# Kernel tuning notes

Measured on AMD Instinct MI355X. Metric: run time of the kernel, lower is better.

Reference implementation:

```python
import jax, jax.numpy as jnp
import numpy as np

N_SEGMENT = 16
N_HEADS = 12
DIM = 768
HEAD_DIM = DIM // N_HEADS
LN_EPS = 1e-5


def setup_inputs() -> dict:
    key = jax.random.key(0)
    ks = jax.random.split(key, 12)
    nt, p, c = 512, 197, DIM
    s = 1.0 / np.sqrt(c)
    return {
        "x": jax.random.normal(ks[0], (nt, p, c), dtype=jnp.float32),
        "w1": jax.random.uniform(ks[1], (1, 1, c), dtype=jnp.float32) * 2.0 - 1.0,
        "ln_g": jnp.ones((c,), dtype=jnp.float32),
        "ln_b": jnp.zeros((c,), dtype=jnp.float32),
        "Wq": jax.random.normal(ks[2], (c, c), dtype=jnp.float32) * s,
        "bq": jax.random.normal(ks[3], (c,), dtype=jnp.float32) * 0.02,
        "Wk": jax.random.normal(ks[4], (c, c), dtype=jnp.float32) * s,
        "bk": jax.random.normal(ks[5], (c,), dtype=jnp.float32) * 0.02,
        "Wv": jax.random.normal(ks[6], (c, c), dtype=jnp.float32) * s,
        "bv": jax.random.normal(ks[7], (c,), dtype=jnp.float32) * 0.02,
        "Wo": jax.random.normal(ks[8], (c, c), dtype=jnp.float32) * s,
        "bo": jax.random.normal(ks[9], (c,), dtype=jnp.float32) * 0.02,
    }


def _layer_norm(x, g, b):
    mu = jnp.mean(x, axis=-1, keepdims=True)
    var = jnp.mean(jnp.square(x - mu), axis=-1, keepdims=True)
    return (x - mu) * jax.lax.rsqrt(var + LN_EPS) * g + b


def _attention(h, Wq, bq, Wk, bk, Wv, bv, Wo, bo):
    # h: [B, T, C]
    B, T, C = h.shape
    def heads(y):
        return y.reshape(B, T, N_HEADS, HEAD_DIM).transpose(0, 2, 1, 3)
    q = heads(h @ Wq + bq)  # [B, H, T, Dh]
    k = heads(h @ Wk + bk)
    v = heads(h @ Wv + bv)
    scores = jnp.einsum("bhtd,bhsd->bhts", q, k) / jnp.sqrt(jnp.float32(HEAD_DIM))
    probs = jax.nn.softmax(scores, axis=-1)
    ctx = jnp.einsum("bhts,bhsd->bhtd", probs, v)
    ctx = ctx.transpose(0, 2, 1, 3).reshape(B, T, C)
    return ctx @ Wo + bo


def reference(x, w1, ln_g, ln_b, Wq, bq, Wk, bk, Wv, bv, Wo, bo):
    nt, p, c = x.shape
    B = nt // N_SEGMENT
    xr = x.reshape(B, N_SEGMENT, p, c)
    s = xr[:, :, 0]  # CLS tokens [B, T, C]
    # weighted temporal shift (in torch this mutates the view; residual sees it)
    s_shift = s.at[:, 1:].add(s[:, :-1] * w1)
    t = _layer_norm(s_shift, ln_g, ln_b)
    t = _attention(t, Wq, bq, Wk, bk, Wv, bv, Wo, bo)
    t = t + s_shift  # residual uses SHIFTED tokens (aliasing in torch source)
    out = xr.at[:, :, 0].set(t)
    return out.reshape(nt, p, c)
```

## Files before the change

### kernel.cpp

```cpp
#include <hip/hip_runtime.h>
#include <math.h>

typedef __attribute__((ext_vector_type(8))) short short8;
typedef __attribute__((ext_vector_type(4))) float f32x4;
typedef __attribute__((ext_vector_type(4))) unsigned short us4;

constexpr int NSEG = 16;
constexpr int CC   = 768;
constexpr int PP   = 197;
constexpr int NH   = 12;
constexpr int HD   = 64;
constexpr int NT   = 512;
constexpr int MN   = NT * CC;
constexpr float LN_EPS = 1e-5f;

constexpr unsigned CPT  = 196 * CC / 4;
constexpr unsigned TOK4 = PP * CC / 4;
constexpr unsigned ROW4 = CC / 4;
constexpr unsigned W4TOT = (unsigned)NT * CPT;

__device__ inline unsigned short f2bf(float f) {
    unsigned u = __float_as_uint(f);
    u += 0x7fffu + ((u >> 16) & 1u);
    return (unsigned short)(u >> 16);
}

__device__ inline void copy_slice(const float* __restrict__ x, float* __restrict__ out,
                                  unsigned start, unsigned end,
                                  unsigned gthread, unsigned nthreads) {
    const float4* __restrict__ x4 = (const float4*)x;
    float4* __restrict__ o4 = (float4*)out;
    for (unsigned i = start + gthread; i < end; i += nthreads) {
        unsigned t = i / CPT;
        unsigned w = i - t * CPT;
        unsigned idx = t * TOK4 + ROW4 + w;
        o4[idx] = x4[idx];
    }
}

template<bool ADD_RES>
__device__ inline void gemm_tile(const unsigned short* __restrict__ A,
                                 const unsigned short* __restrict__ Bt,
                                 const float* __restrict__ bias,
                                 const float* __restrict__ res,
                                 float* __restrict__ outp,
                                 int by, int bx, size_t orow) {
    int tid  = threadIdx.x;
    int lane = tid & 63, wv = tid >> 6;
    int wr = wv >> 1, wc = wv & 1;
    int l15 = lane & 15, lh = lane >> 4;
    int m0 = by * 64 + wr * 32;
    int n0 = bx * 64 + wc * 32;
    f32x4 acc[2][2] = {};
    const unsigned short* Ar0 = A  + (size_t)(m0 + l15) * CC + lh * 8;
    const unsigned short* Ar1 = Ar0 + 16 * CC;
    const unsigned short* Br0 = Bt + (size_t)(n0 + l15) * CC + lh * 8;
    const unsigned short* Br1 = Br0 + 16 * CC;
    #pragma unroll 4
    for (int k0 = 0; k0 < CC; k0 += 32) {
        short8 a0 = *(const short8*)(Ar0 + k0);
        short8 a1 = *(const short8*)(Ar1 + k0);
        short8 b0 = *(const short8*)(Br0 + k0);
        short8 b1 = *(const short8*)(Br1 + k0);
        acc[0][0] = __builtin_amdgcn_mfma_f32_16x16x32_bf16(a0, b0, acc[0][0], 0, 0, 0);
        acc[0][1] = __builtin_amdgcn_mfma_f32_16x16x32_bf16(a0, b1, acc[0][1], 0, 0, 0);
        acc[1][0] = __builtin_amdgcn_mfma_f32_16x16x32_bf16(a1, b0, acc[1][0], 0, 0, 0);
        acc[1][1] = __builtin_amdgcn_mfma_f32_16x16x32_bf16(a1, b1, acc[1][1], 0, 0, 0);
    }
    #pragma unroll
    for (int mf = 0; mf < 2; ++mf)
        #pragma unroll
        for (int nf = 0; nf < 2; ++nf)
            #pragma unroll
            for (int r = 0; r < 4; ++r) {
                int row = m0 + mf * 16 + lh * 4 + r;
                int col = n0 + nf * 16 + l15;
                float v = acc[mf][nf][r] + bias[col];
                if (ADD_RES) v += res[(size_t)row * CC + col];
                outp[(size_t)row * orow + col] = v;
            }
}

constexpr int K1_LN = NT, K1_CVT = 2304, K1_CPY = 768;
__global__ __launch_bounds__(256) void k1(const float* __restrict__ x, const float* __restrict__ w1,
        const float* __restrict__ g, const float* __restrict__ bln,
        const float* __restrict__ Wq, const float* __restrict__ Wk,
        const float* __restrict__ Wv, const float* __restrict__ Wo,
        float* __restrict__ s_shift, unsigned short* __restrict__ tln,
        unsigned short* __restrict__ wt, float* __restrict__ out,
        unsigned cstart, unsigned cend) {
    __shared__ float smem[32 * 33];
    int bid = blockIdx.x, tid = threadIdx.x;
    if (bid < K1_LN) {
        int r = bid, seg = r & (NSEG - 1);
        float vals[3]; float local = 0.f;
        #pragma unroll
        for (int i = 0; i < 3; ++i) {
            int c = tid + i * 256;
            float v = x[(size_t)r * PP * CC + c];
            if (seg > 0) v += w1[c] * x[(size_t)(r - 1) * PP * CC + c];
            vals[i] = v; local += v;
        }
        smem[tid] = local; __syncthreads();
        for (int off = 128; off > 0; off >>= 1) {
            if (tid < off) smem[tid] += smem[tid + off];
            __syncthreads();
        }
        float mu = smem[0] * (1.0f / CC); __syncthreads();
        float lv = 0.f;
        #pragma unroll
        for (int i = 0; i < 3; ++i) { float d = vals[i] - mu; lv += d * d; }
        smem[tid] = lv; __syncthreads();
        for (int off = 128; off > 0; off >>= 1) {
            if (tid < off) smem[tid] += smem[tid + off];
            __syncthreads();
        }
        float rstd = rsqrtf(smem[0] * (1.0f / CC) + LN_EPS);
        #pragma unroll
        for (int i = 0; i < 3; ++i) {
            int c = tid + i * 256;
            s_shift[(size_t)r * CC + c] = vals[i];
            tln[(size_t)r * CC + c] = f2bf((vals[i] - mu) * rstd * g[c] + bln[c]);
        }
    } else if (bid < K1_LN + K1_CVT) {
        int idx = bid - K1_LN;
        int mat = idx / 576, tile = idx % 576;
        int tr = tile / 24, tc = tile % 24;
        const float* W = mat == 0 ? Wq : mat == 1 ? Wk : mat == 2 ? Wv : Wo;
        int lr = tid >> 3, lc = (tid & 7) * 4;
        float4 v = *(const float4*)(W + (size_t)(tr * 32 + lr) * CC + tc * 32 + lc);
        smem[lr * 33 + lc + 0] = v.x; smem[lr * 33 + lc + 1] = v.y;
        smem[lr * 33 + lc + 2] = v.z; smem[lr * 33 + lc + 3] = v.w;
        __syncthreads();
        int ln_ = tid >> 3, kc = (tid & 7) * 4;
        us4 o;
        #pragma unroll
        for (int j = 0; j < 4; ++j) o[j] = f2bf(smem[(kc + j) * 33 + ln_]);
        *(us4*)(wt + (size_t)mat * CC * CC + (size_t)(tc * 32 + ln_) * CC + tr * 32 + kc) = o;
    } else {
        unsigned cb = bid - (K1_LN + K1_CVT);
        copy_slice(x, out, cstart, cend, cb * 256 + tid, K1_CPY * 256);
    }
}

constexpr int K2_GEMM = 288, K2_CPY = 1024;
__global__ __launch_bounds__(256) void k2(const unsigned short* __restrict__ tln,
        const unsigned short* __restrict__ wt,
        const float* __restrict__ bq, const float* __restrict__ bk, const float* __restrict__ bv,
        float* __restrict__ qkv,
        const float* __restrict__ x, float* __restrict__ out,
        unsigned cstart, unsigned cend) {
    int bid = blockIdx.x, tid = threadIdx.x;
    if (bid < K2_GEMM) {
        int z = bid / 96, rem = bid % 96;
        int by = rem / 12, bx = rem % 12;
        const unsigned short* Bt = wt + (size_t)z * CC * CC;
        const float* bias = z == 0 ? bq : (z == 1 ? bk : bv);
        float* outp = qkv + (size_t)z * MN;
        gemm_tile<false>(tln, Bt, bias, nullptr, outp, by, bx, CC);
    } else {
        unsigned cb = bid - K2_GEMM;
        copy_slice(x, out, cstart, cend, cb * 256 + tid, K2_CPY * 256);
    }
}

constexpr int K3_ATT = 32 * NH, K3_CPY = 1024;
__global__ __launch_bounds__(256) void k3(const float* __restrict__ qkv,
        unsigned short* __restrict__ ctxb,
        const float* __restrict__ x, float* __restrict__ out,
        unsigned cstart, unsigned cend) {
    int bid = blockIdx.x, tid = threadIdx.x;
    if (bid < K3_ATT) {
        const float* q = qkv;
        const float* k = qkv + MN;
        const float* v = qkv + 2 * MN;
        int bb = bid / NH, h = bid % NH;
        __shared__ float qs[16][HD], ks[16][HD], vs[16][HD];
        __shared__ float sc[16][17];
        __shared__ float rsum[16];
        for (int i = tid; i < 16 * HD; i += 256) {
            int t = i >> 6, d = i & 63;
            size_t gidx = (size_t)(bb * NSEG + t) * CC + h * HD + d;
            qs[t][d] = q[gidx]; ks[t][d] = k[gidx]; vs[t][d] = v[gidx];
        }
        __syncthreads();
        {
            int t = tid >> 4, s = tid & 15;
            float acc = 0.f;
            #pragma unroll
            for (int d = 0; d < HD; ++d) acc += qs[t][d] * ks[s][d];
            sc[t][s] = acc * 0.125f;
        }
        __syncthreads();
        if (tid < 16) {
            float m = -1e30f;
            #pragma unroll
            for (int s = 0; s < 16; ++s) m = fmaxf(m, sc[tid][s]);
            float sum = 0.f;
            #pragma unroll
            for (int s = 0; s < 16; ++s) { float e = __expf(sc[tid][s] - m); sc[tid][s] = e; sum += e; }
            rsum[tid] = sum;
        }
        __syncthreads();
        for (int i = tid; i < 16 * HD; i += 256) {
            int t = i >> 6, d = i & 63;
            float acc = 0.f;
            #pragma unroll
            for (int s = 0; s < 16; ++s) acc += sc[t][s] * vs[s][d];
            ctxb[(size_t)(bb * NSEG + t) * CC + h * HD + d] = f2bf(acc / rsum[t]);
        }
    } else {
        unsigned cb = bid - K3_ATT;
        copy_slice(x, out, cstart, cend, cb * 256 + tid, K3_CPY * 256);
    }
}

constexpr int K4_GEMM = 96, K4_CPY = 1024;
__global__ __launch_bounds__(256) void k4(const unsigned short* __restrict__ ctxb,
        const unsigned short* __restrict__ wto,
        const float* __restrict__ bo, const float* __restrict__ s_shift,
        float* __restrict__ out, const float* __restrict__ x,
        unsigned cstart, unsigned cend) {
    int bid = blockIdx.x, tid = threadIdx.x;
    if (bid < K4_GEMM) {
        int by = bid / 12, bx = bid % 12;
        gemm_tile<true>(ctxb, wto, bo, s_shift, out, by, bx, (size_t)PP * CC);
    } else {
        unsigned cb = bid - K4_GEMM;
        copy_slice(x, out, cstart, cend, cb * 256 + tid, K4_CPY * 256);
    }
}

extern "C" void kernel_launch(void* const* d_in, const int* in_sizes, int n_in,
                              void* d_out, int out_size, void* d_ws, size_t ws_size,
                              hipStream_t stream) {
    const float* x    = (const float*)d_in[0];
    const float* w1   = (const float*)d_in[1];
    const float* ln_g = (const float*)d_in[2];
    const float* ln_b = (const float*)d_in[3];
    const float* Wq   = (const float*)d_in[4];
    const float* bq   = (const float*)d_in[5];
    const float* Wk   = (const float*)d_in[6];
    const float* bk   = (const float*)d_in[7];
    const float* Wv   = (const float*)d_in[8];
    const float* bv   = (const float*)d_in[9];
    const float* Wo   = (const float*)d_in[10];
    const float* bo   = (const float*)d_in[11];
    float* out = (float*)d_out;

    float* ws      = (float*)d_ws;
    float* s_shift = ws;
    float* qkv     = s_shift + MN;
    unsigned short* tln  = (unsigned short*)(qkv + 3 * MN);
    unsigned short* ctxb = tln + MN;
    unsigned short* wt   = ctxb + MN;

    const unsigned s0 = 0, s1 = 5400000u, s2 = 10400000u, s3 = 15400000u, s4 = W4TOT;

    k1<<<K1_LN + K1_CVT + K1_CPY, 256, 0, stream>>>(x, w1, ln_g, ln_b, Wq, Wk, Wv, Wo,
                                                    s_shift, tln, wt, out, s0, s1);
    k2<<<K2_GEMM + K2_CPY, 256, 0, stream>>>(tln, wt, bq, bk, bv, qkv, x, out, s1, s2);
    k3<<<K3_ATT + K3_CPY, 256, 0, stream>>>(qkv, ctxb, x, out, s2, s3);
    k4<<<K4_GEMM + K4_CPY, 256, 0, stream>>>(ctxb, wt + (size_t)3 * CC * CC, bo, s_shift,
                                             out, x, s3, s4);
}
```

Before: 159.7 us.

## Fuse attention with output projection, unroll copy, and rebalance copy slices

```diff
diff --git a/kernel.cpp b/kernel.cpp
--- a/kernel.cpp
+++ b/kernel.cpp
@@ -25,26 +25,34 @@
     return (unsigned short)(u >> 16);
 }
 
-__device__ inline void copy_slice(const float* __restrict__ x, float* __restrict__ out,
+__device__ inline unsigned cidx(unsigned i) {
+    unsigned t = i / CPT;
+    return i + t * ROW4 + ROW4;
+}
+
+__device__ inline void copy_slice(const float* __restrict__ xf, float* __restrict__ of,
                                   unsigned start, unsigned end,
-                                  unsigned gthread, unsigned nthreads) {
-    const float4* __restrict__ x4 = (const float4*)x;
-    float4* __restrict__ o4 = (float4*)out;
-    for (unsigned i = start + gthread; i < end; i += nthreads) {
-        unsigned t = i / CPT;
-        unsigned w = i - t * CPT;
-        unsigned idx = t * TOK4 + ROW4 + w;
-        o4[idx] = x4[idx];
-    }
-}
-
-template<bool ADD_RES>
+                                  unsigned gt, unsigned nth) {
+    const float4* __restrict__ x4 = (const float4*)xf;
+    float4* __restrict__ o4 = (float4*)of;
+    unsigned i = start + gt;
+    unsigned s1 = nth, s2 = 2 * nth, s3 = 3 * nth, s4 = 4 * nth;
+    for (; i + s3 < end; i += s4) {
+        unsigned a0 = cidx(i), a1 = cidx(i + s1), a2 = cidx(i + s2), a3 = cidx(i + s3);
+        float4 v0 = x4[a0];
+        float4 v1 = x4[a1];
+        float4 v2 = x4[a2];
+        float4 v3 = x4[a3];
+        o4[a0] = v0; o4[a1] = v1; o4[a2] = v2; o4[a3] = v3;
+    }
+    for (; i < end; i += s1) { unsigned a = cidx(i); o4[a] = x4[a]; }
+}
+
 __device__ inline void gemm_tile(const unsigned short* __restrict__ A,
                                  const unsigned short* __restrict__ Bt,
                                  const float* __restrict__ bias,
-                                 const float* __restrict__ res,
                                  float* __restrict__ outp,
-                                 int by, int bx, size_t orow) {
+                                 int by, int bx) {
     int tid  = threadIdx.x;
     int lane = tid & 63, wv = tid >> 6;
     int wr = wv >> 1, wc = wv & 1;
@@ -75,13 +83,11 @@
             for (int r = 0; r < 4; ++r) {
                 int row = m0 + mf * 16 + lh * 4 + r;
                 int col = n0 + nf * 16 + l15;
-                float v = acc[mf][nf][r] + bias[col];
-                if (ADD_RES) v += res[(size_t)row * CC + col];
-                outp[(size_t)row * orow + col] = v;
+                outp[(size_t)row * CC + col] = acc[mf][nf][r] + bias[col];
             }
 }
 
-constexpr int K1_LN = NT, K1_CVT = 2304, K1_CPY = 768;
+constexpr int K1_CPY = 1536, K1_LN = NT, K1_CVT = 2304;
 __global__ __launch_bounds__(256) void k1(const float* __restrict__ x, const float* __restrict__ w1,
         const float* __restrict__ g, const float* __restrict__ bln,
         const float* __restrict__ Wq, const float* __restrict__ Wk,
@@ -91,8 +97,10 @@
         unsigned cstart, unsigned cend) {
     __shared__ float smem[32 * 33];
     int bid = blockIdx.x, tid = threadIdx.x;
-    if (bid < K1_LN) {
-        int r = bid, seg = r & (NSEG - 1);
+    if (bid < K1_CPY) {
+        copy_slice(x, out, cstart, cend, (unsigned)bid * 256 + tid, K1_CPY * 256);
+    } else if (bid < K1_CPY + K1_LN) {
+        int r = bid - K1_CPY, seg = r & (NSEG - 1);
         float vals[3]; float local = 0.f;
         #pragma unroll
         for (int i = 0; i < 3; ++i) {
@@ -122,8 +130,8 @@
             s_shift[(size_t)r * CC + c] = vals[i];
             tln[(size_t)r * CC + c] = f2bf((vals[i] - mu) * rstd * g[c] + bln[c]);
         }
-    } else if (bid < K1_LN + K1_CVT) {
-        int idx = bid - K1_LN;
+    } else {
+        int idx = bid - K1_CPY - K1_LN;
         int mat = idx / 576, tile = idx % 576;
         int tr = tile / 24, tc = tile % 24;
         const float* W = mat == 0 ? Wq : mat == 1 ? Wk : mat == 2 ? Wv : Wo;
@@ -137,13 +145,10 @@
         #pragma unroll
         for (int j = 0; j < 4; ++j) o[j] = f2bf(smem[(kc + j) * 33 + ln_]);
         *(us4*)(wt + (size_t)mat * CC * CC + (size_t)(tc * 32 + ln_) * CC + tr * 32 + kc) = o;
-    } else {
-        unsigned cb = bid - (K1_LN + K1_CVT);
-        copy_slice(x, out, cstart, cend, cb * 256 + tid, K1_CPY * 256);
-    }
-}
-
-constexpr int K2_GEMM = 288, K2_CPY = 1024;
+    }
+}
+
+constexpr int K2_CPY = 1792, K2_GEMM = 288;
 __global__ __launch_bounds__(256) void k2(const unsigned short* __restrict__ tln,
         const unsigned short* __restrict__ wt,
         const float* __restrict__ bq, const float* __restrict__ bk, const float* __restrict__ bv,
@@ -151,44 +156,56 @@
         const float* __restrict__ x, float* __restrict__ out,
         unsigned cstart, unsigned cend) {
     int bid = blockIdx.x, tid = threadIdx.x;
-    if (bid < K2_GEMM) {
-        int z = bid / 96, rem = bid % 96;
+    if (bid < K2_CPY) {
+        copy_slice(x, out, cstart, cend, (unsigned)bid * 256 + tid, K2_CPY * 256);
+    } else {
+        int idx = bid - K2_CPY;
+        int z = idx / 96, rem = idx % 96;
         int by = rem / 12, bx = rem % 12;
-        const unsigned short* Bt = wt + (size_t)z * CC * CC;
         const float* bias = z == 0 ? bq : (z == 1 ? bk : bv);
-        float* outp = qkv + (size_t)z * MN;
-        gemm_tile<false>(tln, Bt, bias, nullptr, outp, by, bx, CC);
-    } else {
-        unsigned cb = bid - K2_GEMM;
-        copy_slice(x, out, cstart, cend, cb * 256 + tid, K2_CPY * 256);
-    }
-}
-
-constexpr int K3_ATT = 32 * NH, K3_CPY = 1024;
+        gemm_tile(tln, wt + (size_t)z * CC * CC, bias, qkv + (size_t)z * MN, by, bx);
+    }
+}
+
+constexpr int K3_CPY = 1792, K3_FUSE = 32;
 __global__ __launch_bounds__(256) void k3(const float* __restrict__ qkv,
-        unsigned short* __restrict__ ctxb,
-        const float* __restrict__ x, float* __restrict__ out,
+        const unsigned short* __restrict__ wto,
+        const float* __restrict__ bo, const float* __restrict__ s_shift,
+        unsigned short* __restrict__ ctxg,
+        float* __restrict__ out, const float* __restrict__ x,
         unsigned cstart, unsigned cend) {
+    __shared__ float qs[16][68], ks[16][68], vs[16][68];
+    __shared__ float sc[16][17];
+    __shared__ float rsum[16];
     int bid = blockIdx.x, tid = threadIdx.x;
-    if (bid < K3_ATT) {
-        const float* q = qkv;
-        const float* k = qkv + MN;
-        const float* v = qkv + 2 * MN;
-        int bb = bid / NH, h = bid % NH;
-        __shared__ float qs[16][HD], ks[16][HD], vs[16][HD];
-        __shared__ float sc[16][17];
-        __shared__ float rsum[16];
-        for (int i = tid; i < 16 * HD; i += 256) {
-            int t = i >> 6, d = i & 63;
-            size_t gidx = (size_t)(bb * NSEG + t) * CC + h * HD + d;
-            qs[t][d] = q[gidx]; ks[t][d] = k[gidx]; vs[t][d] = v[gidx];
-        }
+    if (bid < K3_CPY) {
+        copy_slice(x, out, cstart, cend, (unsigned)bid * 256 + tid, K3_CPY * 256);
+        return;
+    }
+    int bb = bid - K3_CPY;
+    const float* qp = qkv;
+    const float* kp = qkv + MN;
+    const float* vp = qkv + 2 * MN;
+    int row = tid >> 4, c4 = tid & 15;
+
+    for (int h = 0; h < NH; ++h) {
+        size_t base = (size_t)(bb * NSEG + row) * CC + h * HD + c4 * 4;
+        float4 q4 = *(const float4*)(qp + base);
+        float4 k4 = *(const float4*)(kp + base);
+        float4 v4 = *(const float4*)(vp + base);
+        *(float4*)&qs[row][c4 * 4] = q4;
+        *(float4*)&ks[row][c4 * 4] = k4;
+        *(float4*)&vs[row][c4 * 4] = v4;
         __syncthreads();
         {
             int t = tid >> 4, s = tid & 15;
             float acc = 0.f;
             #pragma unroll
-            for (int d = 0; d < HD; ++d) acc += qs[t][d] * ks[s][d];
+            for (int d0 = 0; d0 < HD; d0 += 4) {
+                float4 qv = *(const float4*)&qs[t][d0];
+                float4 kv = *(const float4*)&ks[s][d0];
+                acc += qv.x * kv.x + qv.y * kv.y + qv.z * kv.z + qv.w * kv.w;
+            }
             sc[t][s] = acc * 0.125f;
         }
         __syncthreads();
@@ -196,38 +213,51 @@
             float m = -1e30f;
             #pragma unroll
             for (int s = 0; s < 16; ++s) m = fmaxf(m, sc[tid][s]);
-            float sum = 0.f;
-            #pragma unroll
-            for (int s = 0; s < 16; ++s) { float e = __expf(sc[tid][s] - m); sc[tid][s] = e; sum += e; }
-            rsum[tid] = sum;
-        }
-        __syncthreads();
-        for (int i = tid; i < 16 * HD; i += 256) {
-            int t = i >> 6, d = i & 63;
-            float acc = 0.f;
-            #pragma unroll
-            for (int s = 0; s < 16; ++s) acc += sc[t][s] * vs[s][d];
-            ctxb[(size_t)(bb * NSEG + t) * CC + h * HD + d] = f2bf(acc / rsum[t]);
-        }
-    } else {
-        unsigned cb = bid - K3_ATT;
-        copy_slice(x, out, cstart, cend, cb * 256 + tid, K3_CPY * 256);
-    }
-}
-
-constexpr int K4_GEMM = 96, K4_CPY = 1024;
-__global__ __launch_bounds__(256) void k4(const unsigned short* __restrict__ ctxb,
-        const unsigned short* __restrict__ wto,
-        const float* __restrict__ bo, const float* __restrict__ s_shift,
-        float* __restrict__ out, const float* __restrict__ x,
-        unsigned cstart, unsigned cend) {
-    int bid = blockIdx.x, tid = threadIdx.x;
-    if (bid < K4_GEMM) {
-        int by = bid / 12, bx = bid % 12;
-        gemm_tile<true>(ctxb, wto, bo, s_shift, out, by, bx, (size_t)PP * CC);
-    } else {
-        unsigned cb = bid - K4_GEMM;
-        copy_slice(x, out, cstart, cend, cb * 256 + tid, K4_CPY * 256);
+            float su = 0.f;
+            #pragma unroll
+            for (int s = 0; s < 16; ++s) { float e = __expf(sc[tid][s] - m); sc[tid][s] = e; su += e; }
+            rsum[tid] = su;
+        }
+        __syncthreads();
+        {
+            float4 o = {0.f, 0.f, 0.f, 0.f};
+            #pragma unroll
+            for (int ss = 0; ss < 16; ++ss) {
+                float p = sc[row][ss];
+                float4 vv = *(const float4*)&vs[ss][c4 * 4];
+                o.x += p * vv.x; o.y += p * vv.y; o.z += p * vv.z; o.w += p * vv.w;
+            }
+            float inv = 1.f / rsum[row];
+            us4 ob;
+            ob[0] = f2bf(o.x * inv); ob[1] = f2bf(o.y * inv);
+            ob[2] = f2bf(o.z * inv); ob[3] = f2bf(o.w * inv);
+            *(us4*)(ctxg + (size_t)(bb * NSEG + row) * CC + h * HD + c4 * 4) = ob;
+        }
+        __syncthreads();
+    }
+    __threadfence_block();
+    __syncthreads();
+
+    int lane = tid & 63, wv = tid >> 6;
+    int l15 = lane & 15, lh = lane >> 4;
+    const unsigned short* Arow = ctxg + (size_t)(bb * NSEG + l15) * CC + lh * 8;
+    for (int nt_ = wv; nt_ < 48; nt_ += 4) {
+        int n0 = nt_ * 16;
+        const unsigned short* Brow = wto + (size_t)(n0 + l15) * CC + lh * 8;
+        f32x4 acc = {0.f, 0.f, 0.f, 0.f};
+        #pragma unroll 4
+        for (int k0 = 0; k0 < CC; k0 += 32) {
+            short8 a = *(const short8*)(Arow + k0);
+            short8 b = *(const short8*)(Brow + k0);
+            acc = __builtin_amdgcn_mfma_f32_16x16x32_bf16(a, b, acc, 0, 0, 0);
+        }
+        #pragma unroll
+        for (int r = 0; r < 4; ++r) {
+            int drow = lh * 4 + r;
+            int col = n0 + l15;
+            float v = acc[r] + bo[col] + s_shift[(size_t)(bb * NSEG + drow) * CC + col];
+            out[(size_t)(bb * NSEG + drow) * (size_t)(PP * CC) + col] = v;
+        }
     }
 }
 
@@ -252,15 +282,14 @@
     float* s_shift = ws;
     float* qkv     = s_shift + MN;
     unsigned short* tln  = (unsigned short*)(qkv + 3 * MN);
-    unsigned short* ctxb = tln + MN;
-    unsigned short* wt   = ctxb + MN;
-
-    const unsigned s0 = 0, s1 = 5400000u, s2 = 10400000u, s3 = 15400000u, s4 = W4TOT;
-
-    k1<<<K1_LN + K1_CVT + K1_CPY, 256, 0, stream>>>(x, w1, ln_g, ln_b, Wq, Wk, Wv, Wo,
-                                                    s_shift, tln, wt, out, s0, s1);
-    k2<<<K2_GEMM + K2_CPY, 256, 0, stream>>>(tln, wt, bq, bk, bv, qkv, x, out, s1, s2);
-    k3<<<K3_ATT + K3_CPY, 256, 0, stream>>>(qkv, ctxb, x, out, s2, s3);
-    k4<<<K4_GEMM + K4_CPY, 256, 0, stream>>>(ctxb, wt + (size_t)3 * CC * CC, bo, s_shift,
-                                             out, x, s3, s4);
-}
+    unsigned short* ctxg = tln + MN;
+    unsigned short* wt   = ctxg + MN;
+
+    const unsigned S1 = 3500000u, S2 = 11500000u;
+
+    k1<<<K1_CPY + K1_LN + K1_CVT, 256, 0, stream>>>(x, w1, ln_g, ln_b, Wq, Wk, Wv, Wo,
+                                                    s_shift, tln, wt, out, 0u, S1);
+    k2<<<K2_CPY + K2_GEMM, 256, 0, stream>>>(tln, wt, bq, bk, bv, qkv, x, out, S1, S2);
+    k3<<<K3_CPY + K3_FUSE, 256, 0, stream>>>(qkv, wt + (size_t)3 * CC * CC, bo, s_shift,
+                                             ctxg, out, x, S2, W4TOT);
+}
```

Result: slower. 246.1 us (+54.0%).

## Rebalance bulk copy across kernels, store QKV as bf16, batch weight transposes

Applied to the files above, without the earlier changes.

```diff
diff --git a/kernel.cpp b/kernel.cpp
--- a/kernel.cpp
+++ b/kernel.cpp
@@ -15,35 +15,44 @@
 constexpr float LN_EPS = 1e-5f;
 
 constexpr unsigned CPT  = 196 * CC / 4;
-constexpr unsigned TOK4 = PP * CC / 4;
 constexpr unsigned ROW4 = CC / 4;
 constexpr unsigned W4TOT = (unsigned)NT * CPT;
+
+constexpr unsigned L1 = 7077888u;
+constexpr unsigned L2 = 5406720u;
+constexpr unsigned L3 = 4423680u;
+constexpr unsigned L4 = W4TOT - L1 - L2 - L3;
+constexpr unsigned B2 = L1, B3 = L1 + L2, B4 = L1 + L2 + L3;
 
 __device__ inline unsigned short f2bf(float f) {
     unsigned u = __float_as_uint(f);
     u += 0x7fffu + ((u >> 16) & 1u);
     return (unsigned short)(u >> 16);
 }
-
-__device__ inline void copy_slice(const float* __restrict__ x, float* __restrict__ out,
-                                  unsigned start, unsigned end,
-                                  unsigned gthread, unsigned nthreads) {
-    const float4* __restrict__ x4 = (const float4*)x;
-    float4* __restrict__ o4 = (float4*)out;
-    for (unsigned i = start + gthread; i < end; i += nthreads) {
-        unsigned t = i / CPT;
-        unsigned w = i - t * CPT;
-        unsigned idx = t * TOK4 + ROW4 + w;
-        o4[idx] = x4[idx];
-    }
-}
-
-template<bool ADD_RES>
+__device__ inline float bf2f(unsigned short v) {
+    return __uint_as_float((unsigned)v << 16);
+}
+__device__ inline unsigned cidx(unsigned i) {
+    unsigned t = i / CPT;
+    return i + t * ROW4 + ROW4;
+}
+__device__ inline void copy_strided(const float* __restrict__ xf, float* __restrict__ of,
+                                    unsigned base, unsigned len,
+                                    unsigned ct, unsigned nth) {
+    const f32x4* __restrict__ x4 = (const f32x4*)xf;
+    f32x4* __restrict__ o4 = (f32x4*)of;
+    for (unsigned i = ct; i < len; i += nth) {
+        unsigned a = cidx(base + i);
+        o4[a] = x4[a];
+    }
+}
+
+template<bool ADD_RES, bool BF16_OUT>
 __device__ inline void gemm_tile(const unsigned short* __restrict__ A,
                                  const unsigned short* __restrict__ Bt,
                                  const float* __restrict__ bias,
                                  const float* __restrict__ res,
-                                 float* __restrict__ outp,
+                                 float* __restrict__ outf, unsigned short* __restrict__ outb,
                                  int by, int bx, size_t orow) {
     int tid  = threadIdx.x;
     int lane = tid & 63, wv = tid >> 6;
@@ -77,22 +86,40 @@
                 int col = n0 + nf * 16 + l15;
                 float v = acc[mf][nf][r] + bias[col];
                 if (ADD_RES) v += res[(size_t)row * CC + col];
-                outp[(size_t)row * orow + col] = v;
+                if (BF16_OUT) outb[(size_t)row * orow + col] = f2bf(v);
+                else          outf[(size_t)row * orow + col] = v;
             }
 }
 
-constexpr int K1_LN = NT, K1_CVT = 2304, K1_CPY = 768;
 __global__ __launch_bounds__(256) void k1(const float* __restrict__ x, const float* __restrict__ w1,
         const float* __restrict__ g, const float* __restrict__ bln,
         const float* __restrict__ Wq, const float* __restrict__ Wk,
         const float* __restrict__ Wv, const float* __restrict__ Wo,
         float* __restrict__ s_shift, unsigned short* __restrict__ tln,
-        unsigned short* __restrict__ wt, float* __restrict__ out,
-        unsigned cstart, unsigned cend) {
+        unsigned short* __restrict__ wt, float* __restrict__ out) {
     __shared__ float smem[32 * 33];
     int bid = blockIdx.x, tid = threadIdx.x;
-    if (bid < K1_LN) {
-        int r = bid, seg = r & (NSEG - 1);
+    if (bid < 288) {
+        #pragma unroll
+        for (int rep = 0; rep < 8; ++rep) {
+            int idx = bid + rep * 288;
+            int mat = idx / 576, tile = idx % 576;
+            int tr = tile / 24, tc = tile % 24;
+            const float* W = mat == 0 ? Wq : mat == 1 ? Wk : mat == 2 ? Wv : Wo;
+            int lr = tid >> 3, lc = (tid & 7) * 4;
+            float4 v = *(const float4*)(W + (size_t)(tr * 32 + lr) * CC + tc * 32 + lc);
+            smem[lr * 33 + lc + 0] = v.x; smem[lr * 33 + lc + 1] = v.y;
+            smem[lr * 33 + lc + 2] = v.z; smem[lr * 33 + lc + 3] = v.w;
+            __syncthreads();
+            int ln_ = tid >> 3, kc = (tid & 7) * 4;
+            us4 o;
+            #pragma unroll
+            for (int j = 0; j < 4; ++j) o[j] = f2bf(smem[(kc + j) * 33 + ln_]);
+            *(us4*)(wt + (size_t)mat * CC * CC + (size_t)(tc * 32 + ln_) * CC + tr * 32 + kc) = o;
+            __syncthreads();
+        }
+    } else if (bid < 288 + NT) {
+        int r = bid - 288, seg = r & (NSEG - 1);
         float vals[3]; float local = 0.f;
         #pragma unroll
         for (int i = 0; i < 3; ++i) {
@@ -122,58 +149,35 @@
             s_shift[(size_t)r * CC + c] = vals[i];
             tln[(size_t)r * CC + c] = f2bf((vals[i] - mu) * rstd * g[c] + bln[c]);
         }
-    } else if (bid < K1_LN + K1_CVT) {
-        int idx = bid - K1_LN;
-        int mat = idx / 576, tile = idx % 576;
-        int tr = tile / 24, tc = tile % 24;
-        const float* W = mat == 0 ? Wq : mat == 1 ? Wk : mat == 2 ? Wv : Wo;
-        int lr = tid >> 3, lc = (tid & 7) * 4;
-        float4 v = *(const float4*)(W + (size_t)(tr * 32 + lr) * CC + tc * 32 + lc);
-        smem[lr * 33 + lc + 0] = v.x; smem[lr * 33 + lc + 1] = v.y;
-        smem[lr * 33 + lc + 2] = v.z; smem[lr * 33 + lc + 3] = v.w;
-        __syncthreads();
-        int ln_ = tid >> 3, kc = (tid & 7) * 4;
-        us4 o;
-        #pragma unroll
-        for (int j = 0; j < 4; ++j) o[j] = f2bf(smem[(kc + j) * 33 + ln_]);
-        *(us4*)(wt + (size_t)mat * CC * CC + (size_t)(tc * 32 + ln_) * CC + tr * 32 + kc) = o;
-    } else {
-        unsigned cb = bid - (K1_LN + K1_CVT);
-        copy_slice(x, out, cstart, cend, cb * 256 + tid, K1_CPY * 256);
-    }
-}
-
-constexpr int K2_GEMM = 288, K2_CPY = 1024;
+    }
+    copy_strided(x, out, 0u, L1, (unsigned)bid * 256 + tid, 2048u * 256);
+}
+
 __global__ __launch_bounds__(256) void k2(const unsigned short* __restrict__ tln,
         const unsigned short* __restrict__ wt,
         const float* __restrict__ bq, const float* __restrict__ bk, const float* __restrict__ bv,
-        float* __restrict__ qkv,
-        const float* __restrict__ x, float* __restrict__ out,
-        unsigned cstart, unsigned cend) {
-    int bid = blockIdx.x, tid = threadIdx.x;
-    if (bid < K2_GEMM) {
+        unsigned short* __restrict__ qkvb,
+        const float* __restrict__ x, float* __restrict__ out) {
+    int bid = blockIdx.x, tid = threadIdx.x;
+    if (bid < 288) {
         int z = bid / 96, rem = bid % 96;
         int by = rem / 12, bx = rem % 12;
-        const unsigned short* Bt = wt + (size_t)z * CC * CC;
         const float* bias = z == 0 ? bq : (z == 1 ? bk : bv);
-        float* outp = qkv + (size_t)z * MN;
-        gemm_tile<false>(tln, Bt, bias, nullptr, outp, by, bx, CC);
+        gemm_tile<false, true>(tln, wt + (size_t)z * CC * CC, bias, nullptr,
+                               nullptr, qkvb + (size_t)z * MN, by, bx, CC);
     } else {
-        unsigned cb = bid - K2_GEMM;
-        copy_slice(x, out, cstart, cend, cb * 256 + tid, K2_CPY * 256);
-    }
-}
-
-constexpr int K3_ATT = 32 * NH, K3_CPY = 1024;
-__global__ __launch_bounds__(256) void k3(const float* __restrict__ qkv,
+        copy_strided(x, out, B2, L2, (unsigned)(bid - 288) * 256 + tid, 1760u * 256);
+    }
+}
+
+__global__ __launch_bounds__(256) void k3(const unsigned short* __restrict__ qkvb,
         unsigned short* __restrict__ ctxb,
-        const float* __restrict__ x, float* __restrict__ out,
-        unsigned cstart, unsigned cend) {
-    int bid = blockIdx.x, tid = threadIdx.x;
-    if (bid < K3_ATT) {
-        const float* q = qkv;
-        const float* k = qkv + MN;
-        const float* v = qkv + 2 * MN;
+        const float* __restrict__ x, float* __restrict__ out) {
+    int bid = blockIdx.x, tid = threadIdx.x;
+    if (bid < 384) {
+        const unsigned short* qb = qkvb;
+        const unsigned short* kb = qkvb + MN;
+        const unsigned short* vb = qkvb + 2 * MN;
         int bb = bid / NH, h = bid % NH;
         __shared__ float qs[16][HD], ks[16][HD], vs[16][HD];
         __shared__ float sc[16][17];
@@ -181,7 +185,7 @@
         for (int i = tid; i < 16 * HD; i += 256) {
             int t = i >> 6, d = i & 63;
             size_t gidx = (size_t)(bb * NSEG + t) * CC + h * HD + d;
-            qs[t][d] = q[gidx]; ks[t][d] = k[gidx]; vs[t][d] = v[gidx];
+            qs[t][d] = bf2f(qb[gidx]); ks[t][d] = bf2f(kb[gidx]); vs[t][d] = bf2f(vb[gidx]);
         }
         __syncthreads();
         {
@@ -210,24 +214,20 @@
             ctxb[(size_t)(bb * NSEG + t) * CC + h * HD + d] = f2bf(acc / rsum[t]);
         }
     } else {
-        unsigned cb = bid - K3_ATT;
-        copy_slice(x, out, cstart, cend, cb * 256 + tid, K3_CPY * 256);
-    }
-}
-
-constexpr int K4_GEMM = 96, K4_CPY = 1024;
+        copy_strided(x, out, B3, L3, (unsigned)(bid - 384) * 256 + tid, 1664u * 256);
+    }
+}
+
 __global__ __launch_bounds__(256) void k4(const unsigned short* __restrict__ ctxb,
         const unsigned short* __restrict__ wto,
         const float* __restrict__ bo, const float* __restrict__ s_shift,
-        float* __restrict__ out, const float* __restrict__ x,
-        unsigned cstart, unsigned cend) {
-    int bid = blockIdx.x, tid = threadIdx.x;
-    if (bid < K4_GEMM) {
+        float* __restrict__ out, const float* __restrict__ x) {
+    int bid = blockIdx.x, tid = threadIdx.x;
+    if (bid < 96) {
         int by = bid / 12, bx = bid % 12;
-        gemm_tile<true>(ctxb, wto, bo, s_shift, out, by, bx, (size_t)PP * CC);
+        gemm_tile<true, false>(ctxb, wto, bo, s_shift, out, nullptr, by, bx, (size_t)PP * CC);
     } else {
-        unsigned cb = bid - K4_GEMM;
-        copy_slice(x, out, cstart, cend, cb * 256 + tid, K4_CPY * 256);
+        copy_strided(x, out, B4, L4, (unsigned)(bid - 96) * 256 + tid, 1952u * 256);
     }
 }
 
@@ -248,19 +248,14 @@
     const float* bo   = (const float*)d_in[11];
     float* out = (float*)d_out;
 
-    float* ws      = (float*)d_ws;
-    float* s_shift = ws;
-    float* qkv     = s_shift + MN;
-    unsigned short* tln  = (unsigned short*)(qkv + 3 * MN);
-    unsigned short* ctxb = tln + MN;
+    float* s_shift = (float*)d_ws;
+    unsigned short* tln  = (unsigned short*)(s_shift + MN);
+    unsigned short* qkvb = tln + MN;
+    unsigned short* ctxb = qkvb + 3 * (size_t)MN;
     unsigned short* wt   = ctxb + MN;
 
-    const unsigned s0 = 0, s1 = 5400000u, s2 = 10400000u, s3 = 15400000u, s4 = W4TOT;
-
-    k1<<<K1_LN + K1_CVT + K1_CPY, 256, 0, stream>>>(x, w1, ln_g, ln_b, Wq, Wk, Wv, Wo,
-                                                    s_shift, tln, wt, out, s0, s1);
-    k2<<<K2_GEMM + K2_CPY, 256, 0, stream>>>(tln, wt, bq, bk, bv, qkv, x, out, s1, s2);
-    k3<<<K3_ATT + K3_CPY, 256, 0, stream>>>(qkv, ctxb, x, out, s2, s3);
-    k4<<<K4_GEMM + K4_CPY, 256, 0, stream>>>(ctxb, wt + (size_t)3 * CC * CC, bo, s_shift,
-                                             out, x, s3, s4);
-}
+    k1<<<2048, 256, 0, stream>>>(x, w1, ln_g, ln_b, Wq, Wk, Wv, Wo, s_shift, tln, wt, out);
+    k2<<<2048, 256, 0, stream>>>(tln, wt, bq, bk, bv, qkvb, x, out);
+    k3<<<2048, 256, 0, stream>>>(qkvb, ctxb, x, out);
+    k4<<<2048, 256, 0, stream>>>(ctxb, wt + (size_t)3 * CC * CC, bo, s_shift, out, x);
+}
```

After: 147.7 us. 1.08x faster.
